# Performance work log

Hardware: AMD Instinct MI355X
Metric: run time of the kernel (lower is better)

Reference implementation:

```python
import jax, jax.numpy as jnp
import numpy as np

B, S, F, E, K = 4, 1024, 1024, 8, 2
H = 4 * F  # expert hidden dim, hard-coded as features*4 in the module


def setup_inputs() -> dict:
    key = jax.random.key(0)
    ks = jax.random.split(key, 7)
    def xavier(k, shape):
        fan_in, fan_out = shape[-2], shape[-1]
        scale = jnp.sqrt(6.0 / (fan_in + fan_out))
        return jax.random.uniform(k, shape, jnp.float32, -scale, scale)
    return {
        "x": jax.random.normal(ks[0], (B, S, F), jnp.float32),
        "Wg": xavier(ks[1], (F, E)),
        "bg": jnp.zeros((E,), jnp.float32),
        "W1": xavier(ks[2], (E, F, H)),
        "b1": jnp.zeros((E, H), jnp.float32),
        "W2": xavier(ks[3], (E, H, F)),
        "b2": jnp.zeros((E, F), jnp.float32),
    }


def reference(x, Wg, bg, W1, b1, W2, b2):
    # Gating: softmax over experts, keep top-k, renormalize.
    gate_probs = jax.nn.softmax(x @ Wg + bg, axis=-1)              # (b,s,E)
    k = K
    _, top_idx = jax.lax.top_k(gate_probs, k)                       # (b,s,k)
    expert_mask = jax.nn.one_hot(top_idx, gate_probs.shape[-1],
                                 dtype=gate_probs.dtype).sum(-2)    # (b,s,E)
    selected = gate_probs * expert_mask
    selected = selected / (selected.sum(-1, keepdims=True) + 1e-8)
    # Dense all-expert 2-layer MLP (gelu, tanh approximation as in flax nn.gelu).
    h = jax.nn.gelu(jnp.einsum('bsf,efh->bseh', x, W1) + b1)        # (b,s,E,H)
    expert_out = jnp.einsum('bseh,ehf->bsef', h, W2) + b2[None, None]  # (b,s,E,F)
    # Weighted combine over experts with renormalized top-k gates.
    return jnp.einsum('bsef,bse->bsf', expert_out, selected)
```

## Files before the change

### kernel.cpp

```cpp
#include <hip/hip_runtime.h>
#include <hip/hip_bf16.h>

constexpr int Ff = 1024;
constexpr int Ee = 8;
constexpr int Hh = 4096;
constexpr int T  = 4096;
constexpr int MB = 80;

typedef short     bf16x8 __attribute__((ext_vector_type(8)));
typedef float     f32x4  __attribute__((ext_vector_type(4)));
typedef unsigned short u16x8 __attribute__((ext_vector_type(8)));

__device__ __forceinline__ float gelu_fast(float v) {
  const float c2 = 2.0f * 0.7978845608028654f;
  float z2 = c2 * (v + 0.044715f * v * v * v);
  return v / (1.0f + __expf(-z2));
}

__device__ __forceinline__ unsigned short bf16bits(float f) {
  __hip_bfloat16 h = __float2bfloat16(f);
  return *reinterpret_cast<unsigned short*>(&h);
}

__device__ __forceinline__ void gl_lds16(const void* g, void* l) {
  __builtin_amdgcn_global_load_lds(
      (const __attribute__((address_space(1))) unsigned int*)g,
      (__attribute__((address_space(3))) unsigned int*)l, 16, 0, 0);
}

__global__ __launch_bounds__(256) void gating_kernel(
    const float* __restrict__ x, const float* __restrict__ Wg,
    const float* __restrict__ bg, int* __restrict__ cnt,
    int* __restrict__ list, float* __restrict__ wlist) {
  const int wave = threadIdx.x >> 6;
  const int lane = threadIdx.x & 63;
  const int t = blockIdx.x * 4 + wave;
  float acc[Ee] = {0.f,0.f,0.f,0.f,0.f,0.f,0.f,0.f};
  const float* xrow = x + (size_t)t * Ff;
  for (int f0 = 0; f0 < Ff; f0 += 64) {
    float xv = xrow[f0 + lane];
    const float* wrow = Wg + (size_t)(f0 + lane) * Ee;
    float4 w0 = *reinterpret_cast<const float4*>(wrow);
    float4 w1 = *reinterpret_cast<const float4*>(wrow + 4);
    acc[0] += xv * w0.x; acc[1] += xv * w0.y;
    acc[2] += xv * w0.z; acc[3] += xv * w0.w;
    acc[4] += xv * w1.x; acc[5] += xv * w1.y;
    acc[6] += xv * w1.z; acc[7] += xv * w1.w;
  }
#pragma unroll
  for (int e = 0; e < Ee; ++e) {
#pragma unroll
    for (int off = 32; off; off >>= 1) acc[e] += __shfl_xor(acc[e], off);
  }
  if (lane == 0) {
    float l[Ee], m = -1e30f;
#pragma unroll
    for (int e = 0; e < Ee; ++e) { l[e] = acc[e] + bg[e]; m = fmaxf(m, l[e]); }
    float p[Ee], Z = 0.f;
#pragma unroll
    for (int e = 0; e < Ee; ++e) { p[e] = expf(l[e] - m); Z += p[e]; }
#pragma unroll
    for (int e = 0; e < Ee; ++e) p[e] /= Z;
    int i1 = 0; float p1 = p[0];
#pragma unroll
    for (int e = 1; e < Ee; ++e) if (p[e] > p1) { p1 = p[e]; i1 = e; }
    int i2 = -1; float p2 = -1e30f;
#pragma unroll
    for (int e = 0; e < Ee; ++e) if (e != i1 && p[e] > p2) { p2 = p[e]; i2 = e; }
    float denom = p1 + p2 + 1e-8f;
    int pos = atomicAdd(&cnt[i1], 1);
    list[i1 * T + pos] = t; wlist[i1 * T + pos] = p1 / denom;
    pos = atomicAdd(&cnt[i2], 1);
    list[i2 * T + pos] = t; wlist[i2 * T + pos] = p2 / denom;
  }
}

__global__ void prefix_kernel(const int* __restrict__ cnt, int* __restrict__ offs) {
  if (threadIdx.x == 0) {
    int s = 0;
    for (int e = 0; e < Ee; ++e) { offs[e] = s; s += (cnt[e] + 127) & ~127; }
    offs[Ee] = s;
  }
}

__global__ __launch_bounds__(256) void pack_w_kernel(
    const float* __restrict__ src, unsigned short* __restrict__ dst,
    int sN, size_t s_estride, size_t d_estride, int KT) {
  const int e  = blockIdx.z;
  const int nb = blockIdx.x;
  const int kt = blockIdx.y;
  __shared__ float Ts[128][33];
  const int t = threadIdx.x;
  const float* sb = src + (size_t)e * s_estride + (size_t)(kt * 32) * sN + nb * 128;
  {
    const int row = t >> 5;
    const int cc  = (t & 31) * 4;
#pragma unroll
    for (int i = 0; i < 4; ++i) {
      float4 v = *reinterpret_cast<const float4*>(sb + (size_t)(row + 8 * i) * sN + cc);
      Ts[cc + 0][row + 8 * i] = v.x;
      Ts[cc + 1][row + 8 * i] = v.y;
      Ts[cc + 2][row + 8 * i] = v.z;
      Ts[cc + 3][row + 8 * i] = v.w;
    }
  }
  __syncthreads();
  unsigned short* db = dst + (size_t)e * d_estride + ((size_t)nb * KT + kt) * 4096;
#pragma unroll
  for (int j = 0; j < 2; ++j) {
    const int idx = t + 256 * j;
    const int col = idx & 127, kb = idx >> 7;
    u16x8 o;
#pragma unroll
    for (int q = 0; q < 8; ++q) o[q] = bf16bits(Ts[col][kb * 8 + q]);
    *reinterpret_cast<u16x8*>(db + kb * 1024 + col * 8) = o;
  }
}

__global__ __launch_bounds__(256) void pack_x_kernel(
    const float* __restrict__ x, const int* __restrict__ cnt,
    const int* __restrict__ offs, const int* __restrict__ list,
    unsigned short* __restrict__ xg) {
  const int kt = blockIdx.x;
  const int mb = blockIdx.y;
  const int t = threadIdx.x;
  const int m0g = mb * 128;
  int e = 0;
#pragma unroll
  for (int i = 1; i < Ee; ++i) e += (m0g >= offs[i]) ? 1 : 0;
  const int ce = cnt[e];
  const int row = t >> 1, half = t & 1;
  const int mloc = m0g - offs[e] + row;
  const bool valid = (mloc >= 0) && (mloc < ce);
  const int token = valid ? list[e * T + mloc] : 0;
  const float* sp = x + (size_t)token * Ff + kt * 32 + half * 16;
  u16x8 o0, o1;
#pragma unroll
  for (int i = 0; i < 2; ++i) {
    float4 v = valid ? *reinterpret_cast<const float4*>(sp + i * 4)
                     : make_float4(0.f, 0.f, 0.f, 0.f);
    o0[i * 4 + 0] = bf16bits(v.x); o0[i * 4 + 1] = bf16bits(v.y);
    o0[i * 4 + 2] = bf16bits(v.z); o0[i * 4 + 3] = bf16bits(v.w);
  }
#pragma unroll
  for (int i = 2; i < 4; ++i) {
    float4 v = valid ? *reinterpret_cast<const float4*>(sp + i * 4)
                     : make_float4(0.f, 0.f, 0.f, 0.f);
    o1[(i - 2) * 4 + 0] = bf16bits(v.x); o1[(i - 2) * 4 + 1] = bf16bits(v.y);
    o1[(i - 2) * 4 + 2] = bf16bits(v.z); o1[(i - 2) * 4 + 3] = bf16bits(v.w);
  }
  unsigned short* db = xg + ((size_t)mb * (Ff / 32) + kt) * 4096 + row * 8;
  *reinterpret_cast<u16x8*>(db + (half * 2 + 0) * 1024) = o0;
  *reinterpret_cast<u16x8*>(db + (half * 2 + 1) * 1024) = o1;
}

__global__ __launch_bounds__(256, 3) void gemm1_mfma(
    const unsigned short* __restrict__ xg, const unsigned short* __restrict__ W1P,
    const float* __restrict__ b1, const int* __restrict__ cnt,
    const int* __restrict__ offs, unsigned short* __restrict__ hp, int Hc, int c) {
  const int nxg = Hc >> 7;
  const int nwg = nxg * MB;
  const int raw = blockIdx.x;
  int bid = (raw & 7) * (nwg >> 3) + (raw >> 3);
  const int bw = (nxg >= 4) ? 4 : nxg;
  const int band = bid / (MB * bw);
  const int r2 = bid % (MB * bw);
  const int by = r2 / bw;
  const int bx = band * bw + (r2 % bw);

  const int m0g = by * 128;
  int e = 0;
#pragma unroll
  for (int i = 1; i < Ee; ++i) e += (m0g >= offs[i]) ? 1 : 0;
  const int ce = cnt[e];
  const int mloc = m0g - offs[e];
  if (mloc >= ce) return;
  const int n0 = bx * 128;

  __shared__ __align__(16) unsigned short SMEM[24576];
  unsigned short* AsF = SMEM;
  unsigned short* BsF = SMEM + 12288;

  const int tid = threadIdx.x;
  const int w = tid >> 6, lane = tid & 63;
  const int g = lane >> 4, r16 = lane & 15;
  const int wr = w >> 1, wc = w & 1;

  constexpr int NT = Ff / 32;
  const unsigned short* aU = xg  + (size_t)by * NT * 4096;
  const unsigned short* bU = W1P + (size_t)(e * nxg + bx) * NT * 4096;

  f32x4 acc[4][4] = {};
  auto STAGE = [&](int buf, int kt) {
    const unsigned short* aS = aU + (size_t)kt * 4096 + w * 1024 + lane * 8;
    const unsigned short* bS = bU + (size_t)kt * 4096 + w * 1024 + lane * 8;
    unsigned short* aD = AsF + buf * 4096 + w * 1024;
    unsigned short* bD = BsF + buf * 4096 + w * 1024;
    gl_lds16(aS,       aD);
    gl_lds16(aS + 512, aD + 512);
    gl_lds16(bS,       bD);
    gl_lds16(bS + 512, bD + 512);
  };
  STAGE(0, 0); STAGE(1, 1); STAGE(2, 2);
  int cur = 0;
#pragma unroll 1
  for (int t = 0; t < NT; ++t) {
    const int rem = NT - t;
    if (rem >= 3)      asm volatile("s_waitcnt vmcnt(8)" ::: "memory");
    else if (rem == 2) asm volatile("s_waitcnt vmcnt(4)" ::: "memory");
    else               asm volatile("s_waitcnt vmcnt(0)" ::: "memory");
    __builtin_amdgcn_s_barrier();
    asm volatile("" ::: "memory");
    bf16x8 af[4], bfr[4];
#pragma unroll
    for (int i = 0; i < 4; ++i) {
      af[i]  = *reinterpret_cast<const bf16x8*>(
          AsF + cur * 4096 + g * 1024 + (wr * 64 + i * 16 + r16) * 8);
      bfr[i] = *reinterpret_cast<const bf16x8*>(
          BsF + cur * 4096 + g * 1024 + (wc * 64 + i * 16 + r16) * 8);
    }
    asm volatile("s_waitcnt lgkmcnt(0)" ::: "memory");
    __builtin_amdgcn_sched_barrier(0);
    __builtin_amdgcn_s_barrier();
    if (t + 3 < NT) STAGE(cur, t + 3);
    __builtin_amdgcn_s_setprio(1);
#pragma unroll
    for (int mi = 0; mi < 4; ++mi)
#pragma unroll
      for (int ni = 0; ni < 4; ++ni)
        acc[mi][ni] = __builtin_amdgcn_mfma_f32_16x16x32_bf16(
            af[mi], bfr[ni], acc[mi][ni], 0, 0, 0);
    __builtin_amdgcn_s_setprio(0);
    asm volatile("" ::: "memory");
    cur = (cur == 2) ? 0 : cur + 1;
  }
  __builtin_amdgcn_s_barrier();
  unsigned short (*Ls)[136] = reinterpret_cast<unsigned short(*)[136]>(SMEM);
#pragma unroll
  for (int ni = 0; ni < 4; ++ni) {
    const int col = wc * 64 + ni * 16 + r16;
    const float bias = b1[(size_t)e * Hh + (size_t)c * Hc + n0 + col];
#pragma unroll
    for (int mi = 0; mi < 4; ++mi)
#pragma unroll
      for (int r = 0; r < 4; ++r) {
        const int row = wr * 64 + mi * 16 + g * 4 + r;
        Ls[row][col] = bf16bits(gelu_fast(acc[mi][ni][r] + bias));
      }
  }
  __builtin_amdgcn_s_barrier();
  unsigned short* hb2 = hp + (size_t)by * (Hc >> 5) * 4096 + (size_t)(n0 >> 5) * 4096;
#pragma unroll
  for (int p = 0; p < 8; ++p) {
    const int u = p * 256 + tid;
    const int oct = u >> 7;
    const int row = u & 127;
    const int lc = oct * 8;
    unsigned short* dst = hb2 + ((size_t)((lc >> 5) * 4 + ((lc >> 3) & 3))) * 1024 + row * 8;
    *reinterpret_cast<u16x8*>(dst) = *reinterpret_cast<const u16x8*>(&Ls[row][lc]);
  }
}

__global__ __launch_bounds__(256, 3) void gemm2_mfma(
    const unsigned short* __restrict__ hp, const unsigned short* __restrict__ W2P,
    const float* __restrict__ b2, const int* __restrict__ cnt,
    const int* __restrict__ offs, const int* __restrict__ list,
    const float* __restrict__ wlist, float* __restrict__ out,
    int Hc, int kLen, int ksplit, int biasC) {
  constexpr int nxg = Ff >> 7;
  const int nwg = nxg * MB * ksplit;
  const int raw = blockIdx.x;
  int bid = (raw & 7) * (nwg >> 3) + (raw >> 3);
  const int bx = bid % nxg;
  const int rest = bid / nxg;
  const int by = rest % MB;
  const int bz = rest / MB;

  const int m0g = by * 128;
  int e = 0;
#pragma unroll
  for (int i = 1; i < Ee; ++i) e += (m0g >= offs[i]) ? 1 : 0;
  const int ce = cnt[e];
  const int mloc = m0g - offs[e];
  if (mloc >= ce) return;
  const int n0 = bx * 128;

  __shared__ __align__(16) unsigned short AsF[3 * 4096];
  __shared__ __align__(16) unsigned short BsF[3 * 4096];

  const int tid = threadIdx.x;
  const int w = tid >> 6, lane = tid & 63;
  const int g = lane >> 4, r16 = lane & 15;
  const int wr = w >> 1, wc = w & 1;

  const int KT2 = Hc >> 5;
  const int ktOff = (bz * kLen) >> 5;
  const int NT = kLen >> 5;
  const unsigned short* aU = hp  + ((size_t)by * KT2 + ktOff) * 4096;
  const unsigned short* bU = W2P + ((size_t)(e * nxg + bx) * KT2 + ktOff) * 4096;

  f32x4 acc[4][4] = {};
  auto STAGE = [&](int buf, int kt) {
    const unsigned short* aS = aU + (size_t)kt * 4096 + w * 1024 + lane * 8;
    const unsigned short* bS = bU + (size_t)kt * 4096 + w * 1024 + lane * 8;
    unsigned short* aD = AsF + buf * 4096 + w * 1024;
    unsigned short* bD = BsF + buf * 4096 + w * 1024;
    gl_lds16(aS,       aD);
    gl_lds16(aS + 512, aD + 512);
    gl_lds16(bS,       bD);
    gl_lds16(bS + 512, bD + 512);
  };
  STAGE(0, 0);
  if (NT > 1) STAGE(1, 1);
  if (NT > 2) STAGE(2, 2);
  int cur = 0;
#pragma unroll 1
  for (int t = 0; t < NT; ++t) {
    const int rem = NT - t;
    if (rem >= 3)      asm volatile("s_waitcnt vmcnt(8)" ::: "memory");
    else if (rem == 2) asm volatile("s_waitcnt vmcnt(4)" ::: "memory");
    else               asm volatile("s_waitcnt vmcnt(0)" ::: "memory");
    __builtin_amdgcn_s_barrier();
    asm volatile("" ::: "memory");
    bf16x8 af[4], bfr[4];
#pragma unroll
    for (int i = 0; i < 4; ++i) {
      af[i]  = *reinterpret_cast<const bf16x8*>(
          AsF + cur * 4096 + g * 1024 + (wr * 64 + i * 16 + r16) * 8);
      bfr[i] = *reinterpret_cast<const bf16x8*>(
          BsF + cur * 4096 + g * 1024 + (wc * 64 + i * 16 + r16) * 8);
    }
    asm volatile("s_waitcnt lgkmcnt(0)" ::: "memory");
    __builtin_amdgcn_sched_barrier(0);
    __builtin_amdgcn_s_barrier();
    if (t + 3 < NT) STAGE(cur, t + 3);
    __builtin_amdgcn_s_setprio(1);
#pragma unroll
    for (int mi = 0; mi < 4; ++mi)
#pragma unroll
      for (int ni = 0; ni < 4; ++ni)
        acc[mi][ni] = __builtin_amdgcn_mfma_f32_16x16x32_bf16(
            af[mi], bfr[ni], acc[mi][ni], 0, 0, 0);
    __builtin_amdgcn_s_setprio(0);
    asm volatile("" ::: "memory");
    cur = (cur == 2) ? 0 : cur + 1;
  }
  const bool addBias = (biasC != 0) && (bz == 0);
#pragma unroll
  for (int mi = 0; mi < 4; ++mi)
#pragma unroll
    for (int r = 0; r < 4; ++r) {
      const int row = wr * 64 + mi * 16 + g * 4 + r;
      if (mloc + row >= ce) continue;
      const int token = list[e * T + mloc + row];
      const float wgt = wlist[e * T + mloc + row];
      float* op = out + (size_t)token * Ff;
#pragma unroll
      for (int ni = 0; ni < 4; ++ni) {
        const int col = n0 + wc * 64 + ni * 16 + r16;
        float v = acc[mi][ni][r];
        if (addBias) v += b2[(size_t)e * Ff + col];
        atomicAdd(&op[col], wgt * v);
      }
    }
}

extern "C" void kernel_launch(void* const* d_in, const int* in_sizes, int n_in,
                              void* d_out, int out_size, void* d_ws, size_t ws_size,
                              hipStream_t stream) {
  const float* x  = (const float*)d_in[0];
  const float* Wg = (const float*)d_in[1];
  const float* bg = (const float*)d_in[2];
  const float* W1 = (const float*)d_in[3];
  const float* b1 = (const float*)d_in[4];
  const float* W2 = (const float*)d_in[5];
  const float* b2 = (const float*)d_in[6];
  float* out = (float*)d_out;

  const size_t fixed = 1024 + 2 * (size_t)T * Ee * 4 + (size_t)MB * 128 * Ff * 2;
  int Hc = 4096;
  while (Hc > 256 && fixed + (size_t)Hc * 53248 > ws_size) Hc >>= 1;
  const int nchunk = Hh / Hc;
  const int ksplit = 2;
  const int kLen = Hc / ksplit;

  char* p = (char*)d_ws;
  int*   cnt   = (int*)p;            p += 512;
  int*   offs  = (int*)p;            p += 512;
  int*   list  = (int*)p;            p += (size_t)T * Ee * 4;
  float* wlist = (float*)p;          p += (size_t)T * Ee * 4;
  unsigned short* xg  = (unsigned short*)p;  p += (size_t)MB * 128 * Ff * 2;
  unsigned short* W1P = (unsigned short*)p;  p += (size_t)Ee * Hc * Ff * 2;
  unsigned short* W2P = (unsigned short*)p;  p += (size_t)Ee * Ff * Hc * 2;
  unsigned short* hp  = (unsigned short*)p;

  hipMemsetAsync(d_out, 0, (size_t)out_size * sizeof(float), stream);
  hipMemsetAsync(cnt, 0, 64, stream);

  gating_kernel<<<T / 4, 256, 0, stream>>>(x, Wg, bg, cnt, list, wlist);
  prefix_kernel<<<1, 64, 0, stream>>>(cnt, offs);
  pack_x_kernel<<<dim3(Ff / 32, MB), 256, 0, stream>>>(x, cnt, offs, list, xg);

  for (int c = 0; c < nchunk; ++c) {
    pack_w_kernel<<<dim3(Hc / 128, Ff / 32, Ee), 256, 0, stream>>>(
        W1 + (size_t)c * Hc, W1P, Hh, (size_t)Ff * Hh, (size_t)Hc * Ff, Ff / 32);
    pack_w_kernel<<<dim3(Ff / 128, Hc / 32, Ee), 256, 0, stream>>>(
        W2 + (size_t)c * Hc * Ff, W2P, Ff, (size_t)Hh * Ff, (size_t)Ff * Hc, Hc / 32);
    gemm1_mfma<<<(Hc / 128) * MB, 256, 0, stream>>>(
        xg, W1P, b1, cnt, offs, hp, Hc, c);
    gemm2_mfma<<<(Ff / 128) * MB * ksplit, 256, 0, stream>>>(
        hp, W2P, b2, cnt, offs, list, wlist, out, Hc, kLen, ksplit,
        c == nchunk - 1 ? 1 : 0);
  }
}
```

Measured before the change: 432.5 us.

## Widen GEMM tiles to 128x256 per workgroup in both expert GEMMs

Both MFMA GEMMs now compute 128x256 output tiles instead of 128x128, so each warp holds a 64x128 accumulator block and reuses every A fragment across 8 B fragments. The B staging loads two packed 128-column panels per k-step, with LDS grown to a 3-stage buffer for the wider B tile. Wait counts, the epilogue LDS layout and the grid sizes are adjusted to match. The point is to halve A-tile reloads and raise MFMA work per LDS read, at the cost of more registers, fewer waves per CU (launch bounds dropped to 2), fewer workgroups and the removal of the NT>1/NT>2 guards in gemm2.

```diff
diff --git a/kernel.cpp b/kernel.cpp
--- a/kernel.cpp
+++ b/kernel.cpp
@@ -154,11 +154,11 @@
   *reinterpret_cast<u16x8*>(db + (half * 2 + 1) * 1024) = o1;
 }
 
-__global__ __launch_bounds__(256, 3) void gemm1_mfma(
+__global__ __launch_bounds__(256, 2) void gemm1_mfma(
     const unsigned short* __restrict__ xg, const unsigned short* __restrict__ W1P,
     const float* __restrict__ b1, const int* __restrict__ cnt,
     const int* __restrict__ offs, unsigned short* __restrict__ hp, int Hc, int c) {
-  const int nxg = Hc >> 7;
+  const int nxg = Hc >> 8;
   const int nwg = nxg * MB;
   const int raw = blockIdx.x;
   int bid = (raw & 7) * (nwg >> 3) + (raw >> 3);
@@ -175,9 +175,9 @@
   const int ce = cnt[e];
   const int mloc = m0g - offs[e];
   if (mloc >= ce) return;
-  const int n0 = bx * 128;
-
-  __shared__ __align__(16) unsigned short SMEM[24576];
+  const int n0 = bx * 256;
+
+  __shared__ __align__(16) unsigned short SMEM[36864];
   unsigned short* AsF = SMEM;
   unsigned short* BsF = SMEM + 12288;
 
@@ -187,38 +187,43 @@
   const int wr = w >> 1, wc = w & 1;
 
   constexpr int NT = Ff / 32;
-  const unsigned short* aU = xg  + (size_t)by * NT * 4096;
-  const unsigned short* bU = W1P + (size_t)(e * nxg + bx) * NT * 4096;
-
-  f32x4 acc[4][4] = {};
+  const size_t uStride = (size_t)NT * 4096;
+  const unsigned short* aU = xg  + (size_t)by * uStride;
+  const unsigned short* bU = W1P + (size_t)(e * (Hc >> 7) + bx * 2) * uStride;
+
+  f32x4 acc[4][8] = {};
   auto STAGE = [&](int buf, int kt) {
     const unsigned short* aS = aU + (size_t)kt * 4096 + w * 1024 + lane * 8;
-    const unsigned short* bS = bU + (size_t)kt * 4096 + w * 1024 + lane * 8;
     unsigned short* aD = AsF + buf * 4096 + w * 1024;
-    unsigned short* bD = BsF + buf * 4096 + w * 1024;
     gl_lds16(aS,       aD);
     gl_lds16(aS + 512, aD + 512);
-    gl_lds16(bS,       bD);
-    gl_lds16(bS + 512, bD + 512);
+    const unsigned short* bS = bU + (size_t)(w & 1) * uStride + (size_t)kt * 4096
+                               + (w >> 1) * 2048 + lane * 8;
+    unsigned short* bD = BsF + buf * 8192 + (w & 1) * 4096 + (w >> 1) * 2048;
+    gl_lds16(bS,        bD);
+    gl_lds16(bS + 512,  bD + 512);
+    gl_lds16(bS + 1024, bD + 1024);
+    gl_lds16(bS + 1536, bD + 1536);
   };
   STAGE(0, 0); STAGE(1, 1); STAGE(2, 2);
   int cur = 0;
 #pragma unroll 1
   for (int t = 0; t < NT; ++t) {
     const int rem = NT - t;
-    if (rem >= 3)      asm volatile("s_waitcnt vmcnt(8)" ::: "memory");
-    else if (rem == 2) asm volatile("s_waitcnt vmcnt(4)" ::: "memory");
+    if (rem >= 3)      asm volatile("s_waitcnt vmcnt(12)" ::: "memory");
+    else if (rem == 2) asm volatile("s_waitcnt vmcnt(6)" ::: "memory");
     else               asm volatile("s_waitcnt vmcnt(0)" ::: "memory");
     __builtin_amdgcn_s_barrier();
     asm volatile("" ::: "memory");
-    bf16x8 af[4], bfr[4];
-#pragma unroll
-    for (int i = 0; i < 4; ++i) {
-      af[i]  = *reinterpret_cast<const bf16x8*>(
+    bf16x8 af[4], bfr[8];
+#pragma unroll
+    for (int i = 0; i < 4; ++i)
+      af[i] = *reinterpret_cast<const bf16x8*>(
           AsF + cur * 4096 + g * 1024 + (wr * 64 + i * 16 + r16) * 8);
-      bfr[i] = *reinterpret_cast<const bf16x8*>(
-          BsF + cur * 4096 + g * 1024 + (wc * 64 + i * 16 + r16) * 8);
-    }
+#pragma unroll
+    for (int j = 0; j < 8; ++j)
+      bfr[j] = *reinterpret_cast<const bf16x8*>(
+          BsF + cur * 8192 + wc * 4096 + g * 1024 + (j * 16 + r16) * 8);
     asm volatile("s_waitcnt lgkmcnt(0)" ::: "memory");
     __builtin_amdgcn_sched_barrier(0);
     __builtin_amdgcn_s_barrier();
@@ -227,47 +232,48 @@
 #pragma unroll
     for (int mi = 0; mi < 4; ++mi)
 #pragma unroll
-      for (int ni = 0; ni < 4; ++ni)
-        acc[mi][ni] = __builtin_amdgcn_mfma_f32_16x16x32_bf16(
-            af[mi], bfr[ni], acc[mi][ni], 0, 0, 0);
+      for (int nj = 0; nj < 8; ++nj)
+        acc[mi][nj] = __builtin_amdgcn_mfma_f32_16x16x32_bf16(
+            af[mi], bfr[nj], acc[mi][nj], 0, 0, 0);
     __builtin_amdgcn_s_setprio(0);
     asm volatile("" ::: "memory");
     cur = (cur == 2) ? 0 : cur + 1;
   }
   __builtin_amdgcn_s_barrier();
-  unsigned short (*Ls)[136] = reinterpret_cast<unsigned short(*)[136]>(SMEM);
-#pragma unroll
-  for (int ni = 0; ni < 4; ++ni) {
-    const int col = wc * 64 + ni * 16 + r16;
+  unsigned short* Ls = SMEM;
+#pragma unroll
+  for (int nj = 0; nj < 8; ++nj) {
+    const int col = wc * 128 + nj * 16 + r16;
     const float bias = b1[(size_t)e * Hh + (size_t)c * Hc + n0 + col];
 #pragma unroll
     for (int mi = 0; mi < 4; ++mi)
 #pragma unroll
       for (int r = 0; r < 4; ++r) {
         const int row = wr * 64 + mi * 16 + g * 4 + r;
-        Ls[row][col] = bf16bits(gelu_fast(acc[mi][ni][r] + bias));
+        Ls[row * 264 + col] = bf16bits(gelu_fast(acc[mi][nj][r] + bias));
       }
   }
   __builtin_amdgcn_s_barrier();
-  unsigned short* hb2 = hp + (size_t)by * (Hc >> 5) * 4096 + (size_t)(n0 >> 5) * 4096;
-#pragma unroll
-  for (int p = 0; p < 8; ++p) {
+  const int KT2 = Hc >> 5;
+#pragma unroll
+  for (int p = 0; p < 16; ++p) {
     const int u = p * 256 + tid;
     const int oct = u >> 7;
     const int row = u & 127;
     const int lc = oct * 8;
-    unsigned short* dst = hb2 + ((size_t)((lc >> 5) * 4 + ((lc >> 3) & 3))) * 1024 + row * 8;
-    *reinterpret_cast<u16x8*>(dst) = *reinterpret_cast<const u16x8*>(&Ls[row][lc]);
-  }
-}
-
-__global__ __launch_bounds__(256, 3) void gemm2_mfma(
+    unsigned short* dst = hp + ((size_t)by * KT2 + ((n0 + lc) >> 5)) * 4096 +
+                          ((lc >> 3) & 3) * 1024 + row * 8;
+    *reinterpret_cast<u16x8*>(dst) = *reinterpret_cast<const u16x8*>(&Ls[row * 264 + lc]);
+  }
+}
+
+__global__ __launch_bounds__(256, 2) void gemm2_mfma(
     const unsigned short* __restrict__ hp, const unsigned short* __restrict__ W2P,
     const float* __restrict__ b2, const int* __restrict__ cnt,
     const int* __restrict__ offs, const int* __restrict__ list,
     const float* __restrict__ wlist, float* __restrict__ out,
     int Hc, int kLen, int ksplit, int biasC) {
-  constexpr int nxg = Ff >> 7;
+  constexpr int nxg = Ff >> 8;
   const int nwg = nxg * MB * ksplit;
   const int raw = blockIdx.x;
   int bid = (raw & 7) * (nwg >> 3) + (raw >> 3);
@@ -283,10 +289,11 @@
   const int ce = cnt[e];
   const int mloc = m0g - offs[e];
   if (mloc >= ce) return;
-  const int n0 = bx * 128;
-
-  __shared__ __align__(16) unsigned short AsF[3 * 4096];
-  __shared__ __align__(16) unsigned short BsF[3 * 4096];
+  const int n0 = bx * 256;
+
+  __shared__ __align__(16) unsigned short SMEM[36864];
+  unsigned short* AsF = SMEM;
+  unsigned short* BsF = SMEM + 12288;
 
   const int tid = threadIdx.x;
   const int w = tid >> 6, lane = tid & 63;
@@ -296,40 +303,43 @@
   const int KT2 = Hc >> 5;
   const int ktOff = (bz * kLen) >> 5;
   const int NT = kLen >> 5;
+  const size_t uStride = (size_t)KT2 * 4096;
   const unsigned short* aU = hp  + ((size_t)by * KT2 + ktOff) * 4096;
-  const unsigned short* bU = W2P + ((size_t)(e * nxg + bx) * KT2 + ktOff) * 4096;
-
-  f32x4 acc[4][4] = {};
+  const unsigned short* bU = W2P + ((size_t)(e * (Ff >> 7) + bx * 2) * KT2 + ktOff) * 4096;
+
+  f32x4 acc[4][8] = {};
   auto STAGE = [&](int buf, int kt) {
     const unsigned short* aS = aU + (size_t)kt * 4096 + w * 1024 + lane * 8;
-    const unsigned short* bS = bU + (size_t)kt * 4096 + w * 1024 + lane * 8;
     unsigned short* aD = AsF + buf * 4096 + w * 1024;
-    unsigned short* bD = BsF + buf * 4096 + w * 1024;
     gl_lds16(aS,       aD);
     gl_lds16(aS + 512, aD + 512);
-    gl_lds16(bS,       bD);
-    gl_lds16(bS + 512, bD + 512);
+    const unsigned short* bS = bU + (size_t)(w & 1) * uStride + (size_t)kt * 4096
+                               + (w >> 1) * 2048 + lane * 8;
+    unsigned short* bD = BsF + buf * 8192 + (w & 1) * 4096 + (w >> 1) * 2048;
+    gl_lds16(bS,        bD);
+    gl_lds16(bS + 512,  bD + 512);
+    gl_lds16(bS + 1024, bD + 1024);
+    gl_lds16(bS + 1536, bD + 1536);
   };
-  STAGE(0, 0);
-  if (NT > 1) STAGE(1, 1);
-  if (NT > 2) STAGE(2, 2);
+  STAGE(0, 0); STAGE(1, 1); STAGE(2, 2);
   int cur = 0;
 #pragma unroll 1
   for (int t = 0; t < NT; ++t) {
     const int rem = NT - t;
-    if (rem >= 3)      asm volatile("s_waitcnt vmcnt(8)" ::: "memory");
-    else if (rem == 2) asm volatile("s_waitcnt vmcnt(4)" ::: "memory");
+    if (rem >= 3)      asm volatile("s_waitcnt vmcnt(12)" ::: "memory");
+    else if (rem == 2) asm volatile("s_waitcnt vmcnt(6)" ::: "memory");
     else               asm volatile("s_waitcnt vmcnt(0)" ::: "memory");
     __builtin_amdgcn_s_barrier();
     asm volatile("" ::: "memory");
-    bf16x8 af[4], bfr[4];
-#pragma unroll
-    for (int i = 0; i < 4; ++i) {
-      af[i]  = *reinterpret_cast<const bf16x8*>(
+    bf16x8 af[4], bfr[8];
+#pragma unroll
+    for (int i = 0; i < 4; ++i)
+      af[i] = *reinterpret_cast<const bf16x8*>(
           AsF + cur * 4096 + g * 1024 + (wr * 64 + i * 16 + r16) * 8);
-      bfr[i] = *reinterpret_cast<const bf16x8*>(
-          BsF + cur * 4096 + g * 1024 + (wc * 64 + i * 16 + r16) * 8);
-    }
+#pragma unroll
+    for (int j = 0; j < 8; ++j)
+      bfr[j] = *reinterpret_cast<const bf16x8*>(
+          BsF + cur * 8192 + wc * 4096 + g * 1024 + (j * 16 + r16) * 8);
     asm volatile("s_waitcnt lgkmcnt(0)" ::: "memory");
     __builtin_amdgcn_sched_barrier(0);
     __builtin_amdgcn_s_barrier();
@@ -338,9 +348,9 @@
 #pragma unroll
     for (int mi = 0; mi < 4; ++mi)
 #pragma unroll
-      for (int ni = 0; ni < 4; ++ni)
-        acc[mi][ni] = __builtin_amdgcn_mfma_f32_16x16x32_bf16(
-            af[mi], bfr[ni], acc[mi][ni], 0, 0, 0);
+      for (int nj = 0; nj < 8; ++nj)
+        acc[mi][nj] = __builtin_amdgcn_mfma_f32_16x16x32_bf16(
+            af[mi], bfr[nj], acc[mi][nj], 0, 0, 0);
     __builtin_amdgcn_s_setprio(0);
     asm volatile("" ::: "memory");
     cur = (cur == 2) ? 0 : cur + 1;
@@ -356,9 +366,9 @@
       const float wgt = wlist[e * T + mloc + row];
       float* op = out + (size_t)token * Ff;
 #pragma unroll
-      for (int ni = 0; ni < 4; ++ni) {
-        const int col = n0 + wc * 64 + ni * 16 + r16;
-        float v = acc[mi][ni][r];
+      for (int nj = 0; nj < 8; ++nj) {
+        const int col = n0 + wc * 128 + nj * 16 + r16;
+        float v = acc[mi][nj][r];
         if (addBias) v += b2[(size_t)e * Ff + col];
         atomicAdd(&op[col], wgt * v);
       }
@@ -406,9 +416,9 @@
         W1 + (size_t)c * Hc, W1P, Hh, (size_t)Ff * Hh, (size_t)Hc * Ff, Ff / 32);
     pack_w_kernel<<<dim3(Ff / 128, Hc / 32, Ee), 256, 0, stream>>>(
         W2 + (size_t)c * Hc * Ff, W2P, Ff, (size_t)Hh * Ff, (size_t)Ff * Hc, Hc / 32);
-    gemm1_mfma<<<(Hc / 128) * MB, 256, 0, stream>>>(
+    gemm1_mfma<<<(Hc / 256) * MB, 256, 0, stream>>>(
         xg, W1P, b1, cnt, offs, hp, Hc, c);
-    gemm2_mfma<<<(Ff / 128) * MB * ksplit, 256, 0, stream>>>(
+    gemm2_mfma<<<(Ff / 256) * MB * ksplit, 256, 0, stream>>>(
         hp, W2P, b2, cnt, offs, list, wlist, out, Hc, kLen, ksplit,
         c == nchunk - 1 ? 1 : 0);
   }
```

Result: slower. 481.3 us (+11.3%).
